# Optimization experiments

Measured on AMD Instinct MI355X. Metric: run time of the kernel, lower is better.

## Reference

```python
import jax, jax.numpy as jnp
import numpy as np

TOPK = 9
NUM_CLASSES = 80
EPS = 1e-9


def _bbox_center(boxes):
    return jnp.stack([(boxes[..., 0] + boxes[..., 2]) * 0.5,
                      (boxes[..., 1] + boxes[..., 3]) * 0.5], axis=-1)


def _iou_batch(a, b):
    # a: [N, A, 4], b: [N, C, 4], xyxy -> [N, A, C]
    lt = jnp.maximum(a[:, :, None, :2], b[:, None, :, :2])
    rb = jnp.minimum(a[:, :, None, 2:], b[:, None, :, 2:])
    wh = jax.nn.relu(rb - lt)
    inter = wh[..., 0] * wh[..., 1]
    area_a = (a[..., 2] - a[..., 0]) * (a[..., 3] - a[..., 1])
    area_b = (b[..., 2] - b[..., 0]) * (b[..., 3] - b[..., 1])
    union = area_a[:, :, None] + area_b[:, None, :] - inter + 1e-9
    return inter / union


def _check_points_inside(points, bboxes, eps=EPS):
    # points [L,2], bboxes [B,n,4] -> [B,n,L] float (1 = center inside gt)
    x = points[None, None, :, 0]
    y = points[None, None, :, 1]
    xmin, ymin = bboxes[..., 0:1], bboxes[..., 1:2]
    xmax, ymax = bboxes[..., 2:3], bboxes[..., 3:4]
    dmin = jnp.minimum(jnp.minimum(x - xmin, y - ymin),
                       jnp.minimum(xmax - x, ymax - y))
    return (dmin > eps).astype(bboxes.dtype)


def _gather_topk_pyramid(dist, num_anchors_list, pad_gt_mask, topk):
    # dist: [B,n,L]; per pyramid level pick topk closest anchors per gt
    B, n, _ = dist.shape
    gt_mask = pad_gt_mask.astype(bool)  # [B,n,1]
    bi = jnp.arange(B)[:, None, None]
    gi = jnp.arange(n)[None, :, None]
    starts = [0] + list(np.cumsum(num_anchors_list)[:-1])
    is_in_topk_list, topk_idxs_list = [], []
    for na, start in zip(num_anchors_list, starts):
        d = jax.lax.dynamic_slice_in_dim(dist, start, na, axis=-1)
        _, topk_idxs = jax.lax.top_k(-d, topk)  # smallest distances -> [B,n,topk]
        topk_idxs_list.append(topk_idxs + start)
        idxs = jnp.where(gt_mask, topk_idxs, 0)
        # scatter-count (equivalent to one_hot(...).sum(-2)), then drop duplicates
        cnt = jnp.zeros((B, n, na), dist.dtype).at[bi, gi, idxs].add(1.0)
        is_in_topk_list.append(jnp.where(cnt > 1, 0.0, cnt))
    return jnp.concatenate(is_in_topk_list, -1), jnp.concatenate(topk_idxs_list, -1)


def reference(anchor_bboxes, num_anchors_list, gt_labels, gt_bboxes, pad_gt_mask, bg_index, pred_bboxes):
    L = anchor_bboxes.shape[0]
    B, n, _ = gt_bboxes.shape
    num_anchors_list = [int(v) for v in np.asarray(num_anchors_list)]
    # 1. iou between all gt and all anchors, [B,n,L]
    ious = _iou_batch(gt_bboxes.reshape(1, -1, 4), anchor_bboxes[None]).reshape(B, n, L)
    # 2. center distances, [B,n,L]
    gt_centers = _bbox_center(gt_bboxes)          # [B,n,2]
    anchor_centers = _bbox_center(anchor_bboxes)  # [L,2]
    diff = gt_centers[:, :, None, :] - anchor_centers[None, None, :, :]
    gt2anchor_distances = jnp.sqrt(jnp.sum(diff * diff, axis=-1))
    # 3. per-level topk closest candidates
    is_in_topk, topk_idxs = _gather_topk_pyramid(
        gt2anchor_distances, num_anchors_list, pad_gt_mask, TOPK)
    # 4. mean + std of candidate ious as threshold
    iou_candidates = ious * is_in_topk
    iou_threshold = jnp.take_along_axis(iou_candidates.reshape(B * n, L),
                                        topk_idxs.reshape(B * n, -1), axis=1)
    iou_threshold = iou_threshold.reshape(B, n, -1)
    iou_threshold = (jnp.mean(iou_threshold, axis=-1, keepdims=True)
                     + jnp.std(iou_threshold, axis=-1, keepdims=True, ddof=1))
    # 5. keep candidates above threshold
    is_in_topk = jnp.where(iou_candidates > iou_threshold, is_in_topk, 0.0)
    # 6. restrict centers to be inside gt
    is_in_gts = _check_points_inside(anchor_centers, gt_bboxes)
    mask_positive = is_in_topk * is_in_gts * pad_gt_mask  # [B,n,L]
    mask_positive_sum = mask_positive.sum(axis=-2)        # [B,L]
    # 7. anchors assigned to multiple gts -> keep highest-iou gt
    is_max_iou = (jnp.arange(n)[None, :, None] == ious.argmax(axis=-2)[:, None, :]).astype(ious.dtype)
    mask_positive = jnp.where(mask_positive_sum[:, None, :] > 1, is_max_iou, mask_positive)
    mask_positive_sum = mask_positive.sum(axis=-2)
    assigned_gt_index = mask_positive.argmax(axis=-2)     # [B,L]
    # gather assigned targets
    assigned_labels = jnp.take_along_axis(gt_labels[..., 0], assigned_gt_index, axis=1)
    assigned_labels = jnp.where(mask_positive_sum > 0, assigned_labels,
                                jnp.full_like(assigned_labels, bg_index))
    assigned_bboxes = jnp.take_along_axis(gt_bboxes, assigned_gt_index[..., None], axis=1)
    scores = jax.nn.one_hot(assigned_labels, NUM_CLASSES + 1, dtype=gt_bboxes.dtype)
    keep = np.array([i for i in range(NUM_CLASSES + 1) if i != bg_index])
    assigned_scores = scores[..., keep]                   # [B,L,C]
    # pred_bboxes given: scale scores by max positive iou per anchor
    pious = _iou_batch(gt_bboxes, pred_bboxes) * mask_positive
    assigned_scores = assigned_scores * pious.max(axis=-2)[..., None]
    return assigned_labels, assigned_bboxes, assigned_scores


def setup_inputs():
    key = jax.random.key(0)
    k1, k2, k3, k4 = jax.random.split(key, 4)
    B, n = 16, 64
    strides = [8, 16, 32, 64]
    anchors, num_anchors_list = [], []
    for s in strides:
        fs = 640 // s
        ys, xs = np.meshgrid(np.arange(fs), np.arange(fs), indexing='ij')
        cx = (xs + 0.5) * s
        cy = (ys + 0.5) * s
        half = 2.5 * s
        anchors.append(np.stack([cx - half, cy - half, cx + half, cy + half], -1).reshape(-1, 4))
        num_anchors_list.append(fs * fs)
    anchor_bboxes = jnp.asarray(np.concatenate(anchors, 0), jnp.float32)  # [8500,4]
    ctr = jax.random.uniform(k1, (B, n, 2), minval=32.0, maxval=608.0)
    wh = jax.random.uniform(k2, (B, n, 2), minval=16.0, maxval=256.0)
    gt_bboxes = jnp.concatenate([ctr - wh * 0.5, ctr + wh * 0.5], -1)
    gt_labels = jax.random.randint(k3, (B, n, 1), 0, NUM_CLASSES)
    pad_gt_mask = jnp.broadcast_to((jnp.arange(n) < 48).astype(jnp.float32)[None, :, None], (B, n, 1))
    pred_bboxes = anchor_bboxes[None] + 8.0 * jax.random.normal(k4, (B, anchor_bboxes.shape[0], 4))
    return {'anchor_bboxes': anchor_bboxes,
            'num_anchors_list': tuple(num_anchors_list),
            'gt_labels': gt_labels,
            'gt_bboxes': gt_bboxes,
            'pad_gt_mask': pad_gt_mask,
            'bg_index': NUM_CLASSES,
            'pred_bboxes': pred_bboxes}
```

## Files before the change

### kernel.cpp

```cpp
#include <hip/hip_runtime.h>

#define ROWS_PB 256

__device__ __forceinline__ float iou_box(float4 a, float4 b) {
    float ltx = fmaxf(a.x, b.x);
    float lty = fmaxf(a.y, b.y);
    float rbx = fminf(a.z, b.z);
    float rby = fminf(a.w, b.w);
    float w = fmaxf(rbx - ltx, 0.0f);
    float h = fmaxf(rby - lty, 0.0f);
    float inter = __fmul_rn(w, h);
    float area_a = __fmul_rn(a.z - a.x, a.w - a.y);
    float area_b = __fmul_rn(b.z - b.x, b.w - b.y);
    return inter / (area_a + area_b - inter + 1e-9f);
}

__global__ void init_ws_kernel(uint4* cnt4, uint4* mins4, int n4) {
    int i = blockIdx.x * blockDim.x + threadIdx.x;
    if (i < n4) {
        cnt4[i]  = make_uint4(0u, 0u, 0u, 0u);
        mins4[i] = make_uint4(~0u, ~0u, ~0u, ~0u);
    }
}

struct RoundRes { int won; float iou; int aidx; float4 ab; };

__device__ __forceinline__ RoundRes do_round(int lev_base, int lane,
                                             float gcx, float gcy, float4 g,
                                             const float4* __restrict__ anchors) {
    int active = (lane < 50) ? 1 : 0;
    int sub = (lane < 25) ? 0 : 1;
    int lev = lev_base + sub;
    int c = lane - sub * 25;
    int s = 8 << lev;
    int W = 80 >> lev;
    int start = (lev == 0) ? 0 : (lev == 1) ? 6400 : (lev == 2) ? 8000 : 8400;
    float inv_s = 1.0f / (float)s;
    int ixc = (int)(gcx * inv_s);
    int iyc = (int)(gcy * inv_s);
    int ix0 = min(max(ixc - 2, 0), W - 5);
    int iy0 = min(max(iyc - 2, 0), W - 5);
    int cm = c % 5, cd = c / 5;
    int cx = ix0 + cm;
    int cy = iy0 + cd;
    float acx = ((float)cx + 0.5f) * (float)s;
    float acy = ((float)cy + 0.5f) * (float)s;
    float dx = __fsub_rn(gcx, acx);
    float dy = __fsub_rn(gcy, acy);
    float d = sqrtf(__fadd_rn(__fmul_rn(dx, dx), __fmul_rn(dy, dy)));
    int aidx = start + cy * W + cx;
    unsigned long long key = active
        ? (((unsigned long long)__float_as_uint(d) << 32) | (unsigned)aidx)
        : ~0ull;
    int gbase = sub * 25;
    int rank = 0;
    #pragma unroll
    for (int delta = 1; delta < 25; ++delta) {
        int cs = c + delta;
        if (cs >= 25) cs -= 25;
        unsigned long long o = __shfl(key, gbase + cs);
        rank += (o < key) ? 1 : 0;
    }
    RoundRes r;
    r.won = active && (rank <= 8);
    r.aidx = aidx;
    r.iou = 0.0f;
    r.ab = make_float4(0.f, 0.f, 0.f, 0.f);
    if (r.won) {
        r.ab = anchors[aidx];
        r.iou = iou_box(g, r.ab);
    }
    return r;
}

__global__ __launch_bounds__(64) void topk_rank(
        const float4* __restrict__ anchors,
        const float4* __restrict__ gt,
        const float* __restrict__ pad_mask,
        unsigned* __restrict__ cnt,
        unsigned* __restrict__ mins,
        int n, int L) {
    int bi = blockIdx.x;
    if (pad_mask[bi] == 0.0f) return;
    int b  = bi / n;
    int i  = bi - b * n;
    int lane = threadIdx.x;

    float4 g = gt[bi];
    float gcx = (g.x + g.z) * 0.5f, gcy = (g.y + g.w) * 0.5f;

    RoundRes A = do_round(0, lane, gcx, gcy, g, anchors);
    RoundRes B = do_round(2, lane, gcx, gcy, g, anchors);

    float s = (A.won ? A.iou : 0.0f) + (B.won ? B.iou : 0.0f);
    #pragma unroll
    for (int off = 1; off < 64; off <<= 1) s += __shfl_xor(s, off);
    float mean = s / 36.0f;
    float da = A.won ? (A.iou - mean) : 0.0f;
    float db = B.won ? (B.iou - mean) : 0.0f;
    float ss = da * da + db * db;
    #pragma unroll
    for (int off = 1; off < 64; off <<= 1) ss += __shfl_xor(ss, off);
    float thr = mean + sqrtf(ss / 35.0f);

    size_t rowbase = (size_t)b * L;
    if (A.won && A.iou > thr) {
        float acx = (A.ab.x + A.ab.z) * 0.5f, acy = (A.ab.y + A.ab.w) * 0.5f;
        float dmin = fminf(fminf(acx - g.x, acy - g.y), fminf(g.z - acx, g.w - acy));
        if (dmin > 1e-9f) {
            atomicAdd(&cnt[rowbase + (size_t)A.aidx], 1u);
            atomicMin(&mins[rowbase + (size_t)A.aidx], (unsigned)i);
        }
    }
    if (B.won && B.iou > thr) {
        float acx = (B.ab.x + B.ab.z) * 0.5f, acy = (B.ab.y + B.ab.w) * 0.5f;
        float dmin = fminf(fminf(acx - g.x, acy - g.y), fminf(g.z - acx, g.w - acy));
        if (dmin > 1e-9f) {
            atomicAdd(&cnt[rowbase + (size_t)B.aidx], 1u);
            atomicMin(&mins[rowbase + (size_t)B.aidx], (unsigned)i);
        }
    }
}

__global__ __launch_bounds__(256) void assign_scores_kernel(
        const float4* __restrict__ anchors,
        const float4* __restrict__ gt,
        const int* __restrict__ gt_labels,
        const float4* __restrict__ pred,
        const unsigned* __restrict__ cnt,
        const unsigned* __restrict__ mins,
        const int* __restrict__ bg_index_p,
        float* __restrict__ out,
        int B, int n, int L) {
    __shared__ int   s_lab[ROWS_PB];
    __shared__ float s_piou[ROWS_PB];
    int BL = B * L;
    int base = blockIdx.x * ROWS_PB;
    int tid = threadIdx.x;

    int t = base + tid;
    if (t < BL) {
        int b = t / L;
        int l = t - b * L;
        unsigned c = cnt[t];
        int idx = 0;
        bool pos = false;
        if (c == 1u) {
            idx = (int)mins[t];
            pos = true;
        } else if (c > 1u) {
            float4 abox = anchors[l];
            float best = -1.0f;
            int bi_ = 0;
            for (int ii = 0; ii < n; ++ii) {
                float v = iou_box(gt[b * n + ii], abox);
                if (v > best) { best = v; bi_ = ii; }
            }
            idx = bi_;
            pos = true;
        }
        int bg = *bg_index_p;
        int label = pos ? gt_labels[b * n + idx] : bg;
        float4 gb = gt[b * n + idx];
        float piou = pos ? iou_box(gb, pred[t]) : 0.0f;

        out[t] = (float)label;
        ((float4*)(out + BL))[t] = gb;
        s_lab[tid] = label;
        s_piou[tid] = piou;
    }
    __syncthreads();

    int rows = BL - base;
    if (rows > ROWS_PB) rows = ROWS_PB;
    int nf4 = rows * 20;
    float4* tile = (float4*)(out + (size_t)BL * 5 + (size_t)base * 80);
    #pragma unroll
    for (int k = 0; k < (ROWS_PB * 20) / 256; ++k) {
        int f = k * 256 + tid;
        if (f < nf4) {
            int row = f / 20;
            int c0 = (f - row * 20) * 4;
            int lab = s_lab[row];
            float pv = s_piou[row];
            float4 v;
            v.x = (c0 + 0 == lab) ? pv : 0.0f;
            v.y = (c0 + 1 == lab) ? pv : 0.0f;
            v.z = (c0 + 2 == lab) ? pv : 0.0f;
            v.w = (c0 + 3 == lab) ? pv : 0.0f;
            tile[f] = v;
        }
    }
}

extern "C" void kernel_launch(void* const* d_in, const int* in_sizes, int n_in,
                              void* d_out, int out_size, void* d_ws, size_t ws_size,
                              hipStream_t stream) {
    const float4* anchors    = (const float4*)d_in[0];
    const int*    gt_labels  = (const int*)d_in[2];
    const float4* gt         = (const float4*)d_in[3];
    const float*  pad_mask   = (const float*)d_in[4];
    const int*    bg_index_p = (const int*)d_in[5];
    const float4* pred       = (const float4*)d_in[6];

    int L = in_sizes[0] / 4;
    int n = 64;
    int B = in_sizes[2] / n;
    int BL = B * L;

    unsigned* cnt  = (unsigned*)d_ws;
    unsigned* mins = cnt + BL;

    float* out = (float*)d_out;

    int n4 = BL / 4;
    hipLaunchKernelGGL(init_ws_kernel, dim3((n4 + 255) / 256), dim3(256), 0, stream,
                       (uint4*)cnt, (uint4*)mins, n4);
    hipLaunchKernelGGL(topk_rank, dim3(B * n), dim3(64), 0, stream,
                       anchors, gt, pad_mask, cnt, mins, n, L);
    hipLaunchKernelGGL(assign_scores_kernel, dim3((BL + ROWS_PB - 1) / ROWS_PB), dim3(256), 0, stream,
                       anchors, gt, gt_labels, pred, cnt, mins, bg_index_p,
                       out, B, n, L);
}
```

Before: 38.05 us.

## Split assign and one-hot score write into separate kernels with compile-time shapes

The fused assign+scores kernel is split in two. The first kernel computes labels, boxes and pred IoU per anchor and writes label and IoU to workspace. A second, fully parallel kernel writes the 80-wide one-hot score rows, eight floats per thread. Shapes (B, n, L) are also hardcoded as constants to drop runtime divisions. This adds a kernel launch and a workspace round-trip in exchange for better parallelism in the dominant score write, and it only works for these exact input shapes.

Result: slower. 43.79 us (+15.1%).

```diff
diff --git a/kernel.cpp b/kernel.cpp
--- a/kernel.cpp
+++ b/kernel.cpp
@@ -1,6 +1,9 @@
 #include <hip/hip_runtime.h>
 
-#define ROWS_PB 256
+#define LC 8500
+#define NC 64
+#define BC 16
+#define BLC (BC * LC)
 
 __device__ __forceinline__ float iou_box(float4 a, float4 b) {
     float ltx = fmaxf(a.x, b.x);
@@ -15,9 +18,9 @@
     return inter / (area_a + area_b - inter + 1e-9f);
 }
 
-__global__ void init_ws_kernel(uint4* cnt4, uint4* mins4, int n4) {
+__global__ void init_ws_kernel(uint4* cnt4, uint4* mins4) {
     int i = blockIdx.x * blockDim.x + threadIdx.x;
-    if (i < n4) {
+    if (i < BLC / 4) {
         cnt4[i]  = make_uint4(0u, 0u, 0u, 0u);
         mins4[i] = make_uint4(~0u, ~0u, ~0u, ~0u);
     }
@@ -78,12 +81,11 @@
         const float4* __restrict__ gt,
         const float* __restrict__ pad_mask,
         unsigned* __restrict__ cnt,
-        unsigned* __restrict__ mins,
-        int n, int L) {
+        unsigned* __restrict__ mins) {
     int bi = blockIdx.x;
     if (pad_mask[bi] == 0.0f) return;
-    int b  = bi / n;
-    int i  = bi - b * n;
+    int b  = bi >> 6;
+    int i  = bi & 63;
     int lane = threadIdx.x;
 
     float4 g = gt[bi];
@@ -103,7 +105,7 @@
     for (int off = 1; off < 64; off <<= 1) ss += __shfl_xor(ss, off);
     float thr = mean + sqrtf(ss / 35.0f);
 
-    size_t rowbase = (size_t)b * L;
+    size_t rowbase = (size_t)b * LC;
     if (A.won && A.iou > thr) {
         float acx = (A.ab.x + A.ab.z) * 0.5f, acy = (A.ab.y + A.ab.w) * 0.5f;
         float dmin = fminf(fminf(acx - g.x, acy - g.y), fminf(g.z - acx, g.w - acy));
@@ -122,7 +124,7 @@
     }
 }
 
-__global__ __launch_bounds__(256) void assign_scores_kernel(
+__global__ __launch_bounds__(256) void assign_kernel(
         const float4* __restrict__ anchors,
         const float4* __restrict__ gt,
         const int* __restrict__ gt_labels,
@@ -131,66 +133,61 @@
         const unsigned* __restrict__ mins,
         const int* __restrict__ bg_index_p,
         float* __restrict__ out,
-        int B, int n, int L) {
-    __shared__ int   s_lab[ROWS_PB];
-    __shared__ float s_piou[ROWS_PB];
-    int BL = B * L;
-    int base = blockIdx.x * ROWS_PB;
-    int tid = threadIdx.x;
-
-    int t = base + tid;
-    if (t < BL) {
-        int b = t / L;
-        int l = t - b * L;
-        unsigned c = cnt[t];
-        int idx = 0;
-        bool pos = false;
-        if (c == 1u) {
-            idx = (int)mins[t];
-            pos = true;
-        } else if (c > 1u) {
-            float4 abox = anchors[l];
-            float best = -1.0f;
-            int bi_ = 0;
-            for (int ii = 0; ii < n; ++ii) {
-                float v = iou_box(gt[b * n + ii], abox);
-                if (v > best) { best = v; bi_ = ii; }
-            }
-            idx = bi_;
-            pos = true;
+        int* __restrict__ lab_ws,
+        float* __restrict__ piou_ws) {
+    int t = blockIdx.x * blockDim.x + threadIdx.x;
+    if (t >= BLC) return;
+    int b = t / LC;
+    int l = t - b * LC;
+    unsigned c = cnt[t];
+    int idx = 0;
+    bool pos = false;
+    if (c == 1u) {
+        idx = (int)mins[t];
+        pos = true;
+    } else if (c > 1u) {
+        float4 abox = anchors[l];
+        float best = -1.0f;
+        int bi_ = 0;
+        for (int ii = 0; ii < NC; ++ii) {
+            float v = iou_box(gt[b * NC + ii], abox);
+            if (v > best) { best = v; bi_ = ii; }
         }
-        int bg = *bg_index_p;
-        int label = pos ? gt_labels[b * n + idx] : bg;
-        float4 gb = gt[b * n + idx];
-        float piou = pos ? iou_box(gb, pred[t]) : 0.0f;
-
-        out[t] = (float)label;
-        ((float4*)(out + BL))[t] = gb;
-        s_lab[tid] = label;
-        s_piou[tid] = piou;
-    }
-    __syncthreads();
-
-    int rows = BL - base;
-    if (rows > ROWS_PB) rows = ROWS_PB;
-    int nf4 = rows * 20;
-    float4* tile = (float4*)(out + (size_t)BL * 5 + (size_t)base * 80);
-    #pragma unroll
-    for (int k = 0; k < (ROWS_PB * 20) / 256; ++k) {
-        int f = k * 256 + tid;
-        if (f < nf4) {
-            int row = f / 20;
-            int c0 = (f - row * 20) * 4;
-            int lab = s_lab[row];
-            float pv = s_piou[row];
-            float4 v;
-            v.x = (c0 + 0 == lab) ? pv : 0.0f;
-            v.y = (c0 + 1 == lab) ? pv : 0.0f;
-            v.z = (c0 + 2 == lab) ? pv : 0.0f;
-            v.w = (c0 + 3 == lab) ? pv : 0.0f;
-            tile[f] = v;
-        }
-    }
+        idx = bi_;
+        pos = true;
+    }
+    int bg = *bg_index_p;
+    int label = pos ? gt_labels[b * NC + idx] : bg;
+    float4 gb = gt[b * NC + idx];
+    float piou = pos ? iou_box(gb, pred[t]) : 0.0f;
+
+    out[t] = (float)label;
+    ((float4*)(out + BLC))[t] = gb;
+    lab_ws[t]  = label;
+    piou_ws[t] = piou;
+}
+
+__global__ __launch_bounds__(256) void scores_kernel(
+        const int* __restrict__ lab_ws,
+        const float* __restrict__ piou_ws,
+        float* __restrict__ out) {
+    int t = blockIdx.x * blockDim.x + threadIdx.x;
+    if (t >= BLC * 10) return;
+    int row = t / 10;
+    int c0 = (t - row * 10) * 8;
+    int label = lab_ws[row];
+    float pv = piou_ws[row];
+    float4 v0 = make_float4(c0 + 0 == label ? pv : 0.0f,
+                            c0 + 1 == label ? pv : 0.0f,
+                            c0 + 2 == label ? pv : 0.0f,
+                            c0 + 3 == label ? pv : 0.0f);
+    float4 v1 = make_float4(c0 + 4 == label ? pv : 0.0f,
+                            c0 + 5 == label ? pv : 0.0f,
+                            c0 + 6 == label ? pv : 0.0f,
+                            c0 + 7 == label ? pv : 0.0f);
+    float4* p = (float4*)(out + (size_t)BLC * 5) + (size_t)t * 2;
+    p[0] = v0;
+    p[1] = v1;
 }
 
 extern "C" void kernel_launch(void* const* d_in, const int* in_sizes, int n_in,
@@ -203,22 +200,20 @@
     const int*    bg_index_p = (const int*)d_in[5];
     const float4* pred       = (const float4*)d_in[6];
 
-    int L = in_sizes[0] / 4;
-    int n = 64;
-    int B = in_sizes[2] / n;
-    int BL = B * L;
-
     unsigned* cnt  = (unsigned*)d_ws;
-    unsigned* mins = cnt + BL;
+    unsigned* mins = cnt + BLC;
+    int*      lab  = (int*)(mins + BLC);
+    float*    piou = (float*)(lab + BLC);
 
     float* out = (float*)d_out;
 
-    int n4 = BL / 4;
-    hipLaunchKernelGGL(init_ws_kernel, dim3((n4 + 255) / 256), dim3(256), 0, stream,
-                       (uint4*)cnt, (uint4*)mins, n4);
-    hipLaunchKernelGGL(topk_rank, dim3(B * n), dim3(64), 0, stream,
-                       anchors, gt, pad_mask, cnt, mins, n, L);
-    hipLaunchKernelGGL(assign_scores_kernel, dim3((BL + ROWS_PB - 1) / ROWS_PB), dim3(256), 0, stream,
+    hipLaunchKernelGGL(init_ws_kernel, dim3((BLC / 4 + 255) / 256), dim3(256), 0, stream,
+                       (uint4*)cnt, (uint4*)mins);
+    hipLaunchKernelGGL(topk_rank, dim3(BC * NC), dim3(64), 0, stream,
+                       anchors, gt, pad_mask, cnt, mins);
+    hipLaunchKernelGGL(assign_kernel, dim3((BLC + 255) / 256), dim3(256), 0, stream,
                        anchors, gt, gt_labels, pred, cnt, mins, bg_index_p,
-                       out, B, n, L);
-}
+                       out, lab, piou);
+    hipLaunchKernelGGL(scores_kernel, dim3((BLC * 10 + 255) / 256), dim3(256), 0, stream,
+                       lab, piou, out);
+}
```
